# Kernel tuning notes

Hardware: AMD Instinct MI355X
Metric: run time of the kernel (lower is better)

The kernel has to match this reference:

```python
import jax, jax.numpy as jnp
import numpy as np

NEG_SLOPE = 0.01
LN_EPS = 1e-5


def leaky_relu(x):
    return jax.nn.leaky_relu(x, NEG_SLOPE)


def layer_norm(x, w, b):
    mu = jnp.mean(x, axis=-1, keepdims=True)
    var = jnp.var(x, axis=-1, keepdims=True)
    return (x - mu) * jax.lax.rsqrt(var + LN_EPS) * w + b


def setup_inputs() -> dict:
    key = jax.random.key(0)
    B, N, IN_DIM, OUT_DIM = 16, 1024, 512, 512
    ks = jax.random.split(key, 12)
    s_in = 1.0 / np.sqrt(IN_DIM)
    s_n = 1.0 / np.sqrt(N)
    return {
        "node_feats": jax.random.normal(ks[0], (B, N, IN_DIM), jnp.float32),
        "adj_matrix": jax.random.uniform(ks[1], (B, N, N), jnp.float32),
        "linear_w": jax.random.uniform(ks[2], (OUT_DIM, IN_DIM), jnp.float32, -s_in, s_in),
        "linear_b": jax.random.uniform(ks[3], (OUT_DIM,), jnp.float32, -s_in, s_in),
        "q_w": jax.random.uniform(ks[4], (N, N), jnp.float32, -s_n, s_n),
        "q_b": jax.random.uniform(ks[5], (N,), jnp.float32, -s_n, s_n),
        "k_w": jax.random.uniform(ks[6], (N, N), jnp.float32, -s_n, s_n),
        "k_b": jax.random.uniform(ks[7], (N,), jnp.float32, -s_n, s_n),
        "v_w": jax.random.uniform(ks[8], (N, N), jnp.float32, -s_n, s_n),
        "v_b": jax.random.uniform(ks[9], (N,), jnp.float32, -s_n, s_n),
        "norm1_w": jnp.ones((N,), jnp.float32),
        "norm1_b": jnp.zeros((N,), jnp.float32),
        "norm2_w": jnp.ones((OUT_DIM,), jnp.float32),
        "norm2_b": jnp.zeros((OUT_DIM,), jnp.float32),
        "edge_weight": jnp.ones((N, N), jnp.float32),
    }


def reference(node_feats, adj_matrix, linear_w, linear_b, q_w, q_b, k_w, k_b,
              v_w, v_b, norm1_w, norm1_b, norm2_w, norm2_b, edge_weight):
    N = edge_weight.shape[0]
    channel_scale = N ** (-0.5)

    # weighted adjacency + symmetric degree normalization (D^-1/2 A D^-1/2)
    W_A = adj_matrix * jax.nn.sigmoid(edge_weight)          # [B,N,N]
    d_inv_sqrt = jnp.power(jnp.sum(W_A, axis=-1), -0.5)     # [B,N]
    d_inv_sqrt = jnp.where(jnp.isinf(d_inv_sqrt), 0.0, d_inv_sqrt)
    W_A = d_inv_sqrt[:, :, None] * W_A * d_inv_sqrt[:, None, :]

    # node projection + channel-wise self-attention
    X = leaky_relu(jnp.einsum('bni,oi->bno', node_feats, linear_w) + linear_b)  # [B,N,O]
    Tx = jnp.swapaxes(X, -1, -2)                             # [B,O,N]
    Tx = layer_norm(Tx, norm1_w, norm1_b)
    q = jnp.einsum('bxh,gh->bxg', Tx, q_w) + q_b
    k = jnp.einsum('bxh,gh->bxg', Tx, k_w) + k_b
    v = leaky_relu(jnp.einsum('bxh,gh->bxg', Tx, v_w) + v_b)
    att = jax.nn.softmax(jnp.einsum('bxh,byh->bxy', q, k) * channel_scale, axis=-1)
    Tx = Tx + jnp.einsum('bxy,byh->bxh', att, v)

    # graph propagation + final norm
    X = jnp.swapaxes(Tx, -1, -2)                             # [B,N,O]
    X = jnp.einsum('bnm,bmo->bno', W_A, X)
    return layer_norm(X, norm2_w, norm2_b)
```

## Files before the change

kernel.cpp:

```cpp
#include <hip/hip_runtime.h>


typedef __bf16 bf16x8 __attribute__((ext_vector_type(8)));
typedef float  f32x4  __attribute__((ext_vector_type(4)));

#define DEV __device__ __forceinline__

DEV float bf2f(unsigned short u) {
  union { unsigned i; float f; } x; x.i = ((unsigned)u) << 16; return x.f;
}
DEV unsigned short f2bf(float f) {
  unsigned u = __float_as_uint(f);
  u += 0x7fffu + ((u >> 16) & 1u);
  return (unsigned short)(u >> 16);
}
DEV float sigmoidf_(float x) { return 1.0f / (1.0f + __expf(-x)); }

DEV float wave_sum(float v) {
#pragma unroll
  for (int o = 32; o > 0; o >>= 1) v += __shfl_xor(v, o, 64);
  return v;
}
DEV float wave_max(float v) {
#pragma unroll
  for (int o = 32; o > 0; o >>= 1) v = fmaxf(v, __shfl_xor(v, o, 64));
  return v;
}

DEV void gload16(const unsigned short* g, unsigned short* l) {
  __builtin_amdgcn_global_load_lds(
      (const __attribute__((address_space(1))) unsigned int*)g,
      (__attribute__((address_space(3))) unsigned int*)l, 16, 0, 0);
}

#define BAR()        asm volatile("s_barrier" ::: "memory")
#define WAIT_VM(n)   asm volatile("s_waitcnt vmcnt(" #n ")" ::: "memory")
#define SB0()        __builtin_amdgcn_sched_barrier(0)

__global__ __launch_bounds__(256) void cast_kernel(const float* __restrict__ in,
                                                   unsigned short* __restrict__ out,
                                                   int n4) {
  int g = blockIdx.x * 256 + threadIdx.x;
  if (g >= n4) return;
  float4 v = *(const float4*)(in + (size_t)g * 4);
  ushort4 o;
  o.x = f2bf(v.x); o.y = f2bf(v.y); o.z = f2bf(v.z); o.w = f2bf(v.w);
  *(ushort4*)(out + (size_t)g * 4) = o;
}

__global__ __launch_bounds__(256) void sigrow_kernel(const float* __restrict__ adj,
                                                     const float* __restrict__ edge,
                                                     float* __restrict__ dis) {
  __shared__ float sh[4];
  size_t row = blockIdx.x;
  int n = (int)(row & 1023);
  const float* ar = adj + row * 1024;
  const float* er = edge + (size_t)n * 1024;
  int c = threadIdx.x * 4;
  float4 a4 = *(const float4*)(ar + c);
  float4 e4 = *(const float4*)(er + c);
  float s = a4.x * sigmoidf_(e4.x) + a4.y * sigmoidf_(e4.y) +
            a4.z * sigmoidf_(e4.z) + a4.w * sigmoidf_(e4.w);
  s = wave_sum(s);
  if ((threadIdx.x & 63) == 0) sh[threadIdx.x >> 6] = s;
  __syncthreads();
  if (threadIdx.x == 0) {
    float t = sh[0] + sh[1] + sh[2] + sh[3];
    dis[row] = t > 0.0f ? rsqrtf(t) : 0.0f;
  }
}

__global__ __launch_bounds__(256) void wa_kernel(const float* __restrict__ adj,
                                                 const float* __restrict__ edge,
                                                 const float* __restrict__ dis,
                                                 unsigned short* __restrict__ wa) {
  size_t g = (size_t)blockIdx.x * 256 + threadIdx.x;
  int m = (int)(g & 255) * 4;
  size_t rest = g >> 8;
  int n = (int)(rest & 1023);
  int b = (int)(rest >> 10);
  float4 a4 = *(const float4*)(adj + rest * 1024 + m);
  float4 e4 = *(const float4*)(edge + (size_t)n * 1024 + m);
  float dn = dis[rest];
  float4 dm = *(const float4*)(dis + (size_t)b * 1024 + m);
  ushort4 o;
  o.x = f2bf(dn * a4.x * sigmoidf_(e4.x) * dm.x);
  o.y = f2bf(dn * a4.y * sigmoidf_(e4.y) * dm.y);
  o.z = f2bf(dn * a4.z * sigmoidf_(e4.z) * dm.z);
  o.w = f2bf(dn * a4.w * sigmoidf_(e4.w) * dm.w);
  *(ushort4*)(wa + g * 4) = o;
}

template <int VPT, bool OUTF32>
__global__ __launch_bounds__(256) void ln_kernel(const unsigned short* __restrict__ in,
                                                 const float* __restrict__ gw,
                                                 const float* __restrict__ gb,
                                                 void* __restrict__ out, int D) {
  __shared__ float sh[8];
  size_t row = blockIdx.x;
  const unsigned short* x = in + row * (size_t)D;
  int base = threadIdx.x * VPT;
  float v[VPT];
  if (VPT == 4) {
    ushort4 u = *(const ushort4*)(x + base);
    v[0] = bf2f(u.x); v[1] = bf2f(u.y); v[2] = bf2f(u.z); v[3] = bf2f(u.w);
  } else {
    ushort2 u = *(const ushort2*)(x + base);
    v[0] = bf2f(u.x); v[1] = bf2f(u.y);
  }
  float s = 0.f, sq = 0.f;
#pragma unroll
  for (int i = 0; i < VPT; i++) { s += v[i]; sq += v[i] * v[i]; }
  s = wave_sum(s); sq = wave_sum(sq);
  if ((threadIdx.x & 63) == 0) { sh[threadIdx.x >> 6] = s; sh[4 + (threadIdx.x >> 6)] = sq; }
  __syncthreads();
  s = sh[0] + sh[1] + sh[2] + sh[3];
  sq = sh[4] + sh[5] + sh[6] + sh[7];
  float mean = s / D;
  float var = sq / D - mean * mean;
  float rs = rsqrtf(fmaxf(var, 0.0f) + 1e-5f);
#pragma unroll
  for (int i = 0; i < VPT; i++) {
    float y = (v[i] - mean) * rs * gw[base + i] + gb[base + i];
    if (OUTF32) ((float*)out)[row * D + base + i] = y;
    else        ((unsigned short*)out)[row * D + base + i] = f2bf(y);
  }
}

__global__ __launch_bounds__(256) void softmax_kernel(const float* __restrict__ in,
                                                      const float* __restrict__ in2,
                                                      unsigned short* __restrict__ out) {
  __shared__ float sh[4];
  size_t row = blockIdx.x;
  const float* x = in + row * 512;
  const float* x2 = in2 + row * 512;
  float2 u = *(const float2*)(x + threadIdx.x * 2);
  float2 u2 = *(const float2*)(x2 + threadIdx.x * 2);
  float a = (u.x + u2.x) * 0.03125f, b = (u.y + u2.y) * 0.03125f;
  float m = wave_max(fmaxf(a, b));
  int wid = threadIdx.x >> 6;
  if ((threadIdx.x & 63) == 0) sh[wid] = m;
  __syncthreads();
  m = fmaxf(fmaxf(sh[0], sh[1]), fmaxf(sh[2], sh[3]));
  __syncthreads();
  float e0 = __expf(a - m), e1 = __expf(b - m);
  float s = wave_sum(e0 + e1);
  if ((threadIdx.x & 63) == 0) sh[wid] = s;
  __syncthreads();
  s = sh[0] + sh[1] + sh[2] + sh[3];
  float inv = 1.0f / s;
  ushort2 o; o.x = f2bf(e0 * inv); o.y = f2bf(e1 * inv);
  *(ushort2*)(out + row * 512 + threadIdx.x * 2) = o;
}

#define MFMA16(d, s0, s1) d = __builtin_amdgcn_mfma_f32_16x16x32_bf16(s0, s1, d, 0, 0, 0)

#define STGA(bi, h, kt) do { \
  gload16(gA + (size_t)((h) * 128) * Kr + (size_t)(kt) * 64, As + (bi) * 16384 + (h) * 8192 + ldst); \
  gload16(gA + (size_t)((h) * 128 + 64) * Kr + (size_t)(kt) * 64, As + (bi) * 16384 + (h) * 8192 + 4096 + ldst); \
} while (0)
#define STGB(bi, h, kt) do { \
  gload16(gB + (size_t)((h) * 128) * Kr + (size_t)(kt) * 64, Bs + (bi) * BSZ + (h) * 8192 + ldst); \
  gload16(gB + (size_t)((h) * 128 + 64) * Kr + (size_t)(kt) * 64, Bs + (bi) * BSZ + (h) * 8192 + 4096 + ldst); \
} while (0)

#define LDA(bi, mh) do { \
  _Pragma("unroll") for (int mf = 0; mf < 4; mf++) { \
    a[mf][0] = *(const bf16x8*)&As[(bi) * 16384 + arow + ((mh) * 4 + mf) * 1024 + xs0]; \
    a[mf][1] = *(const bf16x8*)&As[(bi) * 16384 + arow + ((mh) * 4 + mf) * 1024 + xs1]; \
  } } while (0)
#define LDB(bi, nh) do { \
  if constexpr (BNT == 256) { \
    _Pragma("unroll") for (int nf = 0; nf < 2; nf++) { \
      bb[(nh) * 2 + nf][0] = *(const bf16x8*)&Bs[(bi) * BSZ + brow + ((nh) * 2 + nf) * 1024 + xs0]; \
      bb[(nh) * 2 + nf][1] = *(const bf16x8*)&Bs[(bi) * BSZ + brow + ((nh) * 2 + nf) * 1024 + xs1]; \
    } \
  } else { \
    _Pragma("unroll") for (int nf = 0; nf < 2; nf++) { \
      bb[nf][0] = *(const bf16x8*)&Bs[(bi) * BSZ + brow + nf * 1024 + xs0]; \
      bb[nf][1] = *(const bf16x8*)&Bs[(bi) * BSZ + brow + nf * 1024 + xs1]; \
    } \
  } } while (0)

#define MMQ(mh, nh) do { \
  __builtin_amdgcn_s_setprio(1); \
  if constexpr (BNT == 256) { \
    _Pragma("unroll") for (int mf = 0; mf < 4; mf++) \
    _Pragma("unroll") for (int nf = 0; nf < 2; nf++) { \
      MFMA16(acc[(mh) * 4 + mf][(nh) * 2 + nf], a[mf][0], bb[(nh) * 2 + nf][0]); \
      MFMA16(acc[(mh) * 4 + mf][(nh) * 2 + nf], a[mf][1], bb[(nh) * 2 + nf][1]); \
    } \
  } else { \
    _Pragma("unroll") for (int mf = 0; mf < 4; mf++) { \
      MFMA16(acc[(mh) * 4 + mf][(nh)], a[mf][0], bb[(nh)][0]); \
      MFMA16(acc[(mh) * 4 + mf][(nh)], a[mf][1], bb[(nh)][1]); \
    } \
  } \
  __builtin_amdgcn_s_setprio(0); } while (0)

#define TILE(P, kt, STG, EW) do { \
  EW; BAR(); \
  LDA(P, 0); LDB(P, 0); \
  BAR(); SB0(); MMQ(0, 0); SB0(); BAR(); \
  if constexpr (BNT == 256) { LDB(P, 1); } \
  BAR(); SB0(); MMQ(0, 1); SB0(); BAR(); \
  LDA(P, 1); \
  if (STG) { STGB(P, 0, (kt) + 2); if constexpr (BNT == 256) { STGB(P, 1, (kt) + 2); } } \
  BAR(); SB0(); MMQ(1, 1); SB0(); BAR(); \
  if (STG) { STGA(P, 0, (kt) + 2); STGA(P, 1, (kt) + 2); } \
  BAR(); SB0(); MMQ(1, 0); SB0(); \
} while (0)

template <int BNT, int BIAS , bool LEAKY, bool RESID,
          bool OUTF32, bool SPLIT, bool SPLITK>
__global__ __launch_bounds__(512, 2) void gemm256(
    const unsigned short* __restrict__ A, size_t sA,
    const unsigned short* __restrict__ Bt, size_t sB,
    const float* __restrict__ bias, const float* __restrict__ bias2,
    const unsigned short* __restrict__ resid,
    void* __restrict__ out, void* __restrict__ out2,
    int M, int NcS, int K, int Kst, int lgx, int lgy, int xh) {
  constexpr int NFR = (BNT == 256) ? 4 : 2;
  constexpr int BSZ = BNT * 64;
  __shared__ unsigned short As[2 * 16384];
  __shared__ unsigned short Bs[2 * BSZ];
  const int qc = gridDim.x >> 3;
  const int dd = blockIdx.x;
  const int lb = (dd & 7) * qc + (dd >> 3);
  const int x = lb & ((1 << lgx) - 1);
  const int y = (lb >> lgx) & ((1 << lgy) - 1);
  const int b = (lb >> (lgx + lgy)) & 15;
  const int sk = SPLITK ? (lb >> (lgx + lgy + 4)) : 0;

  const int tid = threadIdx.x;
  const int wid = tid >> 6, lane = tid & 63;
  const int wr = wid >> 2, wc = wid & 3;
  const int l15 = lane & 15, l4 = lane >> 4;
  const int tM = y * 256, tN = x * BNT;
  const size_t Kr = (size_t)Kst;

  const int srow = wid * 8 + (lane >> 3);
  const int scol = ((lane & 7) ^ ((lane >> 3) & 7)) * 8;
  const int koff = sk * K;
  const unsigned short* gA = A + sA * b + (size_t)(tM + srow) * Kr + scol + koff;
  const unsigned short* gB = Bt + sB * b + (size_t)(tN + srow) * Kr + scol + koff;
  const int ldst = wid * 512;

  const int xs0 = ((0 * 4 + l4) ^ (lane & 7)) * 8;
  const int xs1 = ((1 * 4 + l4) ^ (lane & 7)) * 8;
  const int arow = (wr * 128 + l15) * 64;
  const int brow = (wc * (BNT / 4) + l15) * 64;

  f32x4 acc[8][NFR] = {};
  bf16x8 a[4][2], bb[NFR][2];

  const int nt = K >> 6;
  STGB(0, 0, 0);
  if constexpr (BNT == 256) { STGB(0, 1, 0); }
  STGA(0, 0, 0); STGA(0, 1, 0);
  STGB(1, 0, 1);
  if constexpr (BNT == 256) { STGB(1, 1, 1); }
  STGA(1, 0, 1); STGA(1, 1, 1);

  if constexpr (BNT == 256) {
    for (int kt = 0; kt < nt - 2; kt += 2) {
      TILE(0, kt, true, WAIT_VM(8));
      TILE(1, kt + 1, true, WAIT_VM(8));
    }
    TILE(0, nt - 2, false, WAIT_VM(8));
    TILE(1, nt - 1, false, WAIT_VM(0));
  } else {
    for (int kt = 0; kt < nt - 2; kt += 2) {
      TILE(0, kt, true, WAIT_VM(6));
      TILE(1, kt + 1, true, WAIT_VM(6));
    }
    TILE(0, nt - 2, false, WAIT_VM(6));
    TILE(1, nt - 1, false, WAIT_VM(0));
  }

  const float* bia = bias;
  void* o = out;
  if (SPLIT && x >= xh) { bia = bias2; o = out2; }
  if (SPLITK && sk) o = out2;
  const size_t ob = (size_t)M * NcS * b;
#pragma unroll
  for (int mf = 0; mf < 8; mf++)
#pragma unroll
    for (int nf = 0; nf < NFR; nf++) {
      const int cg = tN + wc * (BNT / 4) + nf * 16 + l15;
      const int rbase = tM + wr * 128 + mf * 16 + l4 * 4;
#pragma unroll
      for (int r = 0; r < 4; r++) {
        const int rg = rbase + r;
        float v = acc[mf][nf][r];
        if (BIAS == 1) v += bia[rg];
        if (BIAS == 2) v += bia[cg];
        if (LEAKY) v = v > 0.0f ? v : 0.01f * v;
        const size_t idx = ob + (size_t)rg * NcS + cg;
        if (RESID) v += bf2f(resid[idx]);
        if (OUTF32) ((float*)o)[idx] = v;
        else        ((unsigned short*)o)[idx] = f2bf(v);
      }
    }
}

extern "C" void kernel_launch(void* const* d_in, const int* in_sizes, int n_in,
                              void* d_out, int out_size, void* d_ws, size_t ws_size,
                              hipStream_t stream) {
  const float* node_feats = (const float*)d_in[0];
  const float* adj        = (const float*)d_in[1];
  const float* linear_w   = (const float*)d_in[2];
  const float* linear_b   = (const float*)d_in[3];
  const float* q_w        = (const float*)d_in[4];
  const float* q_b        = (const float*)d_in[5];
  const float* k_w        = (const float*)d_in[6];
  const float* k_b        = (const float*)d_in[7];
  const float* v_w        = (const float*)d_in[8];
  const float* v_b        = (const float*)d_in[9];
  const float* n1w        = (const float*)d_in[10];
  const float* n1b        = (const float*)d_in[11];
  const float* n2w        = (const float*)d_in[12];
  const float* n2b        = (const float*)d_in[13];
  const float* edge       = (const float*)d_in[14];
  float* out = (float*)d_out;

  const int B = 16, N = 1024, C = 512;
  const size_t MiB = 1u << 20;
  char* w = (char*)d_ws;
  unsigned short* nf_bf   = (unsigned short*)(w);
  unsigned short* Xt_bf   = (unsigned short*)(w + 16 * MiB);
  float*          att_raw = (float*)(w);
  float*          att_raw2= (float*)(w + 16 * MiB);
  unsigned short* WA_bf   = (unsigned short*)(w);
  unsigned short* Txln    = (unsigned short*)(w + 32 * MiB);
  unsigned short* q_bf    = (unsigned short*)(w + 48 * MiB);
  unsigned short* X3_bf   = (unsigned short*)(w + 48 * MiB);
  unsigned short* k_bf    = (unsigned short*)(w + 64 * MiB);
  unsigned short* att_bf  = (unsigned short*)(w + 64 * MiB);
  unsigned short* vt_bf   = (unsigned short*)(w + 80 * MiB);
  unsigned short* Tx2_bf  = (unsigned short*)(w + 96 * MiB);
  unsigned short* lw_bf   = (unsigned short*)(w + 112 * MiB);
  unsigned short* qw_bf   = (unsigned short*)(w + 113 * MiB);
  unsigned short* kw_bf   = (unsigned short*)(w + 115 * MiB);
  unsigned short* vw_bf   = (unsigned short*)(w + 117 * MiB);
  float*          dis     = (float*)(w + 119 * MiB);

  cast_kernel<<<(B * N * C / 4 + 255) / 256, 256, 0, stream>>>(node_feats, nf_bf, B * N * C / 4);
  cast_kernel<<<(C * C / 4 + 255) / 256, 256, 0, stream>>>(linear_w, lw_bf, C * C / 4);
  cast_kernel<<<(N * N / 4 + 255) / 256, 256, 0, stream>>>(q_w, qw_bf, N * N / 4);
  cast_kernel<<<(N * N / 4 + 255) / 256, 256, 0, stream>>>(k_w, kw_bf, N * N / 4);
  cast_kernel<<<(N * N / 4 + 255) / 256, 256, 0, stream>>>(v_w, vw_bf, N * N / 4);

  sigrow_kernel<<<B * N, 256, 0, stream>>>(adj, edge, dis);

  gemm256<128, 1, true, false, false, false, false><<<256, 512, 0, stream>>>(
      lw_bf, 0, nf_bf, (size_t)N * C, linear_b, nullptr, nullptr,
      Xt_bf, nullptr, C, N, C, C, 3, 1, 999);

  ln_kernel<4, false><<<B * C, 256, 0, stream>>>(Xt_bf, n1w, n1b, Txln, N);

  gemm256<256, 2, false, false, false, true, false><<<256, 512, 0, stream>>>(
      Txln, (size_t)C * N, qw_bf, 0, q_b, k_b - 1024, nullptr,
      q_bf, (void*)(k_bf - 1024), C, N, N, N, 3, 1, 4);

  gemm256<128, 1, true, false, false, false, false><<<256, 512, 0, stream>>>(
      vw_bf, 0, Txln, (size_t)C * N, v_b, nullptr, nullptr,
      vt_bf, nullptr, N, C, N, N, 2, 2, 999);

  gemm256<128, 0, false, false, true, false, true><<<256, 512, 0, stream>>>(
      q_bf, (size_t)C * N, k_bf, (size_t)C * N, nullptr, nullptr, nullptr,
      att_raw, att_raw2, C, C, 512, N, 2, 1, 999);

  softmax_kernel<<<B * C, 256, 0, stream>>>(att_raw, att_raw2, att_bf);

  wa_kernel<<<B * N * N / 4 / 256, 256, 0, stream>>>(adj, edge, dis, WA_bf);

  gemm256<128, 0, false, true, false, false, false><<<256, 512, 0, stream>>>(
      att_bf, (size_t)C * C, vt_bf, (size_t)N * C, nullptr, nullptr, Txln,
      Tx2_bf, nullptr, C, N, C, C, 3, 1, 999);

  gemm256<128, 0, false, false, false, false, false><<<256, 512, 0, stream>>>(
      WA_bf, (size_t)N * N, Tx2_bf, (size_t)C * N, nullptr, nullptr, nullptr,
      X3_bf, nullptr, N, C, N, N, 2, 2, 999);

  ln_kernel<2, true><<<B * N, 256, 0, stream>>>(X3_bf, n2w, n2b, out, C);
}
```

Baseline: 217.4 us.

## Restructure GEMM K-loop into two MFMA phases with staggered A/B prefetch

Merges the four MFMA quarter-phases per K tile into two half-phases, so each tile needs fewer barriers. A-tile prefetch now runs one tile ahead instead of two, issued into the other buffer, while B keeps a two-tile lookahead. The vmcnt wait thresholds change to match. This cuts barrier and scheduling overhead, but the shorter A prefetch distance leaves less time to hide global-load latency and raises the risk of buffer hazards.

Result: no change. 218.6 us (+0.6%).

```diff
diff --git a/kernel.cpp b/kernel.cpp
--- a/kernel.cpp
+++ b/kernel.cpp
@@ -182,8 +182,7 @@
     } \
   } } while (0)
 
-#define MMQ(mh, nh) do { \
-  __builtin_amdgcn_s_setprio(1); \
+#define MMQB(mh, nh) do { \
   if constexpr (BNT == 256) { \
     _Pragma("unroll") for (int mf = 0; mf < 4; mf++) \
     _Pragma("unroll") for (int nf = 0; nf < 2; nf++) { \
@@ -195,20 +194,22 @@
       MFMA16(acc[(mh) * 4 + mf][(nh)], a[mf][0], bb[(nh)][0]); \
       MFMA16(acc[(mh) * 4 + mf][(nh)], a[mf][1], bb[(nh)][1]); \
     } \
-  } \
+  } } while (0)
+
+#define MMQ2(mh) do { \
+  __builtin_amdgcn_s_setprio(1); \
+  MMQB(mh, 0); MMQB(mh, 1); \
   __builtin_amdgcn_s_setprio(0); } while (0)
 
-#define TILE(P, kt, STG, EW) do { \
+#define TILE2(P, kt, SA, SB, EW) do { \
   EW; BAR(); \
   LDA(P, 0); LDB(P, 0); \
-  BAR(); SB0(); MMQ(0, 0); SB0(); BAR(); \
   if constexpr (BNT == 256) { LDB(P, 1); } \
-  BAR(); SB0(); MMQ(0, 1); SB0(); BAR(); \
+  if (SA) { STGA((P) ^ 1, 0, (kt) + 1); STGA((P) ^ 1, 1, (kt) + 1); } \
+  BAR(); SB0(); MMQ2(0); SB0(); BAR(); \
   LDA(P, 1); \
-  if (STG) { STGB(P, 0, (kt) + 2); if constexpr (BNT == 256) { STGB(P, 1, (kt) + 2); } } \
-  BAR(); SB0(); MMQ(1, 1); SB0(); BAR(); \
-  if (STG) { STGA(P, 0, (kt) + 2); STGA(P, 1, (kt) + 2); } \
-  BAR(); SB0(); MMQ(1, 0); SB0(); \
+  if (SB) { STGB(P, 0, (kt) + 2); if constexpr (BNT == 256) { STGB(P, 1, (kt) + 2); } } \
+  BAR(); SB0(); MMQ2(1); SB0(); \
 } while (0)
 
 template <int BNT, int BIAS , bool LEAKY, bool RESID,
@@ -260,22 +261,21 @@
   STGA(0, 0, 0); STGA(0, 1, 0);
   STGB(1, 0, 1);
   if constexpr (BNT == 256) { STGB(1, 1, 1); }
-  STGA(1, 0, 1); STGA(1, 1, 1);
 
   if constexpr (BNT == 256) {
     for (int kt = 0; kt < nt - 2; kt += 2) {
-      TILE(0, kt, true, WAIT_VM(8));
-      TILE(1, kt + 1, true, WAIT_VM(8));
+      TILE2(0, kt, true, true, WAIT_VM(4));
+      TILE2(1, kt + 1, true, true, WAIT_VM(4));
     }
-    TILE(0, nt - 2, false, WAIT_VM(8));
-    TILE(1, nt - 1, false, WAIT_VM(0));
+    TILE2(0, nt - 2, true, false, WAIT_VM(4));
+    TILE2(1, nt - 1, false, false, WAIT_VM(0));
   } else {
     for (int kt = 0; kt < nt - 2; kt += 2) {
-      TILE(0, kt, true, WAIT_VM(6));
-      TILE(1, kt + 1, true, WAIT_VM(6));
+      TILE2(0, kt, true, true, WAIT_VM(2));
+      TILE2(1, kt + 1, true, true, WAIT_VM(2));
     }
-    TILE(0, nt - 2, false, WAIT_VM(6));
-    TILE(1, nt - 1, false, WAIT_VM(0));
+    TILE2(0, nt - 2, true, false, WAIT_VM(2));
+    TILE2(1, nt - 1, false, false, WAIT_VM(0));
   }
 
   const float* bia = bias;
```
